# Performance work log

Measured on AMD Instinct MI355X. Metric: run time of the kernel, lower is better.

## Reference

```python
import jax, jax.numpy as jnp
import numpy as np

B, S, N, D, H = 128, 512, 32, 512, 2  # batch, seq_len, num_size, node_dim, hop_size
NPAD = 4  # padded number slots per row


def _lin(key, fi, fo):
    return 0.02 * jax.random.normal(key, (H, fi, fo), jnp.float32), jnp.zeros((H, fo), jnp.float32)


def setup_inputs() -> dict:
    key = jax.random.key(0)
    ks = jax.random.split(key, 12)
    encoder_outputs = jax.random.normal(ks[0], (S, B, D), jnp.float32)
    num_encoder_outputs = jax.random.normal(ks[1], (B, N, D), jnp.float32)
    # distinct positions per row in [0, S), last NPAD slots padded with -1
    num_pos_pad = jnp.argsort(jax.random.uniform(ks[2], (B, S)), axis=-1)[:, :N].astype(jnp.int32)
    num_pos_pad = num_pos_pad.at[:, -NPAD:].set(-1)
    # order ranks 1..N (random permutation per row), 0 on padded slots
    num_order_pad = (jnp.argsort(jax.random.uniform(ks[3], (B, N)), axis=-1) + 1).astype(jnp.int32)
    num_order_pad = num_order_pad.at[:, -NPAD:].set(0)
    w_n1a, b_n1a = _lin(ks[4], D, D)
    w_n1b, b_n1b = _lin(ks[5], D, D)
    w_n2a, b_n2a = _lin(ks[6], D, D)
    w_n2b, b_n2b = _lin(ks[7], D, D)
    w_g, b_g = _lin(ks[8], 4 * D, D)
    w_o, b_o = _lin(ks[9], 2 * D, D)
    return dict(encoder_outputs=encoder_outputs, num_encoder_outputs=num_encoder_outputs,
                num_pos_pad=num_pos_pad, num_order_pad=num_order_pad,
                w_n1a=w_n1a, b_n1a=b_n1a, w_n1b=w_n1b, b_n1b=b_n1b,
                w_n2a=w_n2a, b_n2a=b_n2a, w_n2b=w_n2b, b_n2b=b_n2b,
                w_g=w_g, b_g=b_g, w_o=w_o, b_o=b_o)


def reference(encoder_outputs, num_encoder_outputs, num_pos_pad, num_order_pad,
              w_n1a, b_n1a, w_n1b, b_n1b, w_n2a, b_n2a, w_n2b, b_n2b,
              w_g, b_g, w_o, b_o):
    node_mask = (num_order_pad > 0)                              # [B,N]
    greater = num_order_pad[:, :, None] > num_order_pad[:, None, :]
    lower = ~greater                                             # <=
    eye = jnp.eye(N, dtype=jnp.float32)
    pair = (node_mask[:, None, :] & node_mask[:, :, None]).astype(jnp.float32) * (1.0 - eye)
    g_gt = pair * greater.astype(jnp.float32) + eye              # [B,N,N]
    g_lt = pair * lower.astype(jnp.float32) + eye
    # row-normalize (D^{-1} A); diagonal guarantees row sums >= 1
    g_gt = g_gt / g_gt.sum(-1, keepdims=True)
    g_lt = g_lt / g_lt.sum(-1, keepdims=True)

    node = num_encoder_outputs                                   # [B,N,D]
    for h in range(H):
        ni1 = jax.nn.relu(jnp.einsum('bnm,bmd,de->bne', g_gt, node, w_n1a[h]) + b_n1a[h])
        ni1 = jax.nn.relu(jnp.einsum('bnm,bmd,de->bne', g_gt, ni1, w_n1b[h]) + b_n1b[h])
        ni2 = jax.nn.relu(jnp.einsum('bnm,bmd,de->bne', g_lt, node, w_n2a[h]) + b_n2a[h])
        ni2 = jax.nn.relu(jnp.einsum('bnm,bmd,de->bne', g_lt, ni2, w_n2b[h]) + b_n2b[h])
        gate_in = jnp.concatenate([ni1, ni2, ni1 + ni2, ni1 - ni2], axis=-1)
        gate = jax.nn.sigmoid(gate_in @ w_g[h] + b_g[h])
        node_info = gate * ni1 + (1.0 - gate) * ni2
        node = jax.nn.relu(jnp.concatenate([node, node_info], axis=-1) @ w_o[h] + b_o[h])

    # scatter node embeddings into padded [B, S+1, D]; pads -> slot S (dropped)
    num_mask = num_pos_pad > -1
    clamped = jnp.where(num_mask, num_pos_pad, S)                # [B,N]
    gnn_info = jnp.zeros((B, S + 1, D), jnp.float32)
    gnn_info = gnn_info.at[jnp.arange(B)[:, None], clamped].set(node)
    gnn_info = gnn_info[:, :S, :].transpose(1, 0, 2)             # [S,B,D]
    gnn_info = encoder_outputs + gnn_info
    num_embedding = num_encoder_outputs + node
    problem_output = jnp.max(gnn_info, axis=0)                   # [B,D]
    return gnn_info, num_embedding, problem_output
```

## Files before the change

### kernel.cpp

```cpp
#include <hip/hip_runtime.h>
#include <math.h>

#define BB 128
#define SS 512
#define NN 32
#define DD 512
#define HH 2
#define MM (BB * NN)
#define DSQ (DD * DD)

typedef short bf16x8 __attribute__((ext_vector_type(8)));
typedef float f32x4 __attribute__((ext_vector_type(4)));

__device__ __forceinline__ unsigned short f2bf(float f) {
    unsigned int u = __float_as_uint(f);
    u += 0x7fffu + ((u >> 16) & 1u);
    return (unsigned short)(u >> 16);
}
__device__ __forceinline__ float bf2f(unsigned short h) {
    return __uint_as_float(((unsigned int)h) << 16);
}
__device__ __forceinline__ void g2l16(const void* gp, void* lp) {
    __builtin_amdgcn_global_load_lds(
        (const __attribute__((address_space(1))) void*)gp,
        (__attribute__((address_space(3))) void*)lp, 16, 0, 0);
}

__global__ __launch_bounds__(256) void adj_k(const int* __restrict__ order,
                                             const int* __restrict__ pos,
                                             float* __restrict__ g_gt,
                                             float* __restrict__ g_lt,
                                             int* __restrict__ slot) {
    int b = blockIdx.x;
    __shared__ int ord[NN];
    __shared__ float sgt[NN][NN + 1];
    __shared__ float slt[NN][NN + 1];
    __shared__ float rs_gt[NN], rs_lt[NN];
    int tid = threadIdx.x;
    slot[b * SS + tid] = -1;
    slot[b * SS + 256 + tid] = -1;
    if (tid < NN) ord[tid] = order[b * NN + tid];
    __syncthreads();
    for (int q = 0; q < 4; ++q) {
        int idx = tid + 256 * q;
        int n = idx >> 5, m = idx & 31;
        bool valid = (ord[n] > 0) && (ord[m] > 0) && (n != m);
        float eye = (n == m) ? 1.f : 0.f;
        bool gt = ord[n] > ord[m];
        sgt[n][m] = ((valid && gt) ? 1.f : 0.f) + eye;
        slt[n][m] = ((valid && !gt) ? 1.f : 0.f) + eye;
    }
    __syncthreads();
    if (tid < NN) {
        float s1 = 0.f, s2 = 0.f;
        for (int m = 0; m < NN; ++m) { s1 += sgt[tid][m]; s2 += slt[tid][m]; }
        rs_gt[tid] = s1; rs_lt[tid] = s2;
    }
    __syncthreads();
    for (int q = 0; q < 4; ++q) {
        int idx = tid + 256 * q;
        int n = idx >> 5, m = idx & 31;
        g_gt[b * 1024 + idx] = sgt[n][m] / rs_gt[n];
        g_lt[b * 1024 + idx] = slt[n][m] / rs_lt[n];
    }
    if (tid < NN) {
        int p = pos[b * NN + tid];
        if (p >= 0) slot[b * SS + p] = tid;
    }
}

struct WSfull { const float* s[12]; int slot[12]; const float* w_g; };

__global__ __launch_bounds__(256) void wprep_k(WSfull w, unsigned short* __restrict__ Wt) {
    int which = blockIdx.x;
    int tile = blockIdx.y;
    int tr = (tile >> 3) * 64, tc = (tile & 7) * 64;
    __shared__ float c1[64][65];
    __shared__ float c2[64][65];
    int lc = threadIdx.x & 63, g4 = threadIdx.x >> 6;
    if (which < 12) {
        const float* src = w.s[which];
        unsigned short* dst = Wt + (size_t)w.slot[which] * DSQ;
        for (int i = 0; i < 16; ++i) {
            int lr = g4 * 16 + i;
            c1[lr][lc] = src[(size_t)(tr + lr) * DD + tc + lc];
        }
        __syncthreads();
        for (int i = 0; i < 16; ++i) {
            int lr = g4 * 16 + i;
            dst[(size_t)(tc + lr) * DD + tr + lc] = f2bf(c1[lc][lr]);
        }
    } else {
        int h = which - 12;
        const float* base = w.w_g + (size_t)h * 4 * DSQ;
        for (int i = 0; i < 16; ++i) {
            int lr = g4 * 16 + i;
            int k = tr + lr, n = tc + lc;
            float a  = base[(size_t)k * DD + n];
            float b2 = base[(size_t)(DD + k) * DD + n];
            float c  = base[(size_t)(2 * DD + k) * DD + n];
            float d4 = base[(size_t)(3 * DD + k) * DD + n];
            c1[lr][lc] = a + c + d4;
            c2[lr][lc] = b2 + c - d4;
        }
        __syncthreads();
        unsigned short* d1 = Wt + (size_t)(h * 8 + 4) * DSQ;
        unsigned short* d2 = Wt + (size_t)(h * 8 + 5) * DSQ;
        for (int i = 0; i < 16; ++i) {
            int lr = g4 * 16 + i;
            d1[(size_t)(tc + lr) * DD + tr + lc] = f2bf(c1[lc][lr]);
            d2[(size_t)(tc + lr) * DD + tr + lc] = f2bf(c2[lc][lr]);
        }
    }
}

__global__ __launch_bounds__(256) void convmix_k(const float* __restrict__ x,
                                                 const float* __restrict__ g_gt,
                                                 const float* __restrict__ g_lt,
                                                 unsigned short* __restrict__ node0,
                                                 unsigned short* __restrict__ t1,
                                                 unsigned short* __restrict__ t2) {
    const int b = blockIdx.x;
    const int dc = blockIdx.y * 128;
    __shared__ float xs[NN][128];
    __shared__ float gg[2][NN][NN];
    const int t = threadIdx.x;
    ((float4*)gg)[t]       = ((const float4*)(g_gt + (size_t)b * 1024))[t];
    ((float4*)gg)[t + 256] = ((const float4*)(g_lt + (size_t)b * 1024))[t];
#pragma unroll
    for (int q = 0; q < 4; ++q) {
        int e = t + 256 * q;
        int row = e >> 5, c4 = (e & 31) * 4;
        float4 v = *(const float4*)(x + (size_t)(b * NN + row) * DD + dc + c4);
        *(float4*)&xs[row][c4] = v;
        ushort4 o;
        o.x = f2bf(v.x); o.y = f2bf(v.y); o.z = f2bf(v.z); o.w = f2bf(v.w);
        *(ushort4*)(node0 + (size_t)(b * NN + row) * DD + dc + c4) = o;
    }
    __syncthreads();
#pragma unroll
    for (int gi = 0; gi < 2; ++gi) {
        unsigned short* O = gi ? t2 : t1;
#pragma unroll
        for (int it = 0; it < 4; ++it) {
            int task = it * 256 + t;
            int n = task >> 5, dq = task & 31;
            f32x4 r = {0.f, 0.f, 0.f, 0.f};
#pragma unroll
            for (int m = 0; m < NN; ++m)
                r += gg[gi][n][m] * *(const f32x4*)(&xs[m][dq * 4]);
            ushort4 ov;
            ov.x = f2bf(r.x); ov.y = f2bf(r.y); ov.z = f2bf(r.z); ov.w = f2bf(r.w);
            *(ushort4*)(O + (size_t)(b * NN + n) * DD + dc + dq * 4) = ov;
        }
    }
}

struct GA {
    const unsigned short* A1; const unsigned short* W1;
    const unsigned short* A2; const unsigned short* W2;
    const float* bias;
    const unsigned short* gin1; const unsigned short* gin2;
    const float* G1; const float* G2;
    unsigned short* out; unsigned short* out2; unsigned short* out3;
};

template <bool DUAL, bool GATE, int EMIX>
__global__ __launch_bounds__(256) void mgemm_k(GA a0, GA a1) {
    GA g = (blockIdx.z == 0) ? a0 : a1;
    constexpr int LDSB = 49152 + (EMIX == 1 ? 8192 : EMIX == 2 ? 16384 : 0);
    __shared__ __align__(16) char lds[LDSB];
    unsigned short* Ab = (unsigned short*)lds;
    unsigned short* Bb = (unsigned short*)(lds + 16384);
    float* gsh = (float*)(lds + 49152);
    const int tid = threadIdx.x;
    const int lane = tid & 63;
    const int wave = tid >> 6;
    const int wr = wave & 1, wc = wave >> 1;
    const int bm = blockIdx.x * 64, bn = blockIdx.y * 128;

    if (EMIX >= 1) {
        const float4* g1 = (const float4*)(g.G1 + (size_t)(bm >> 5) * 1024);
        ((float4*)gsh)[tid] = g1[tid];
        ((float4*)gsh)[tid + 256] = g1[tid + 256];
        if (EMIX == 2) {
            const float4* g2v = (const float4*)(g.G2 + (size_t)(bm >> 5) * 1024);
            ((float4*)(gsh + 2048))[tid] = g2v[tid];
            ((float4*)(gsh + 2048))[tid + 256] = g2v[tid + 256];
        }
    }

    f32x4 acc[2][4];
#pragma unroll
    for (int i = 0; i < 2; ++i)
#pragma unroll
        for (int j = 0; j < 4; ++j) {
            acc[i][j].x = 0.f; acc[i][j].y = 0.f; acc[i][j].z = 0.f; acc[i][j].w = 0.f;
        }

    const int rA0 = tid >> 3,          sA0 = (tid & 7) ^ (rA0 & 7);
    const int rA1 = (tid + 256) >> 3,  sA1 = (tid & 7) ^ (rA1 & 7);
    int rB[4], sB[4];
#pragma unroll
    for (int q = 0; q < 4; ++q) {
        int e = tid + 256 * q;
        rB[q] = e >> 3;
        sB[q] = (tid & 7) ^ (rB[q] & 7);
    }

    int aoff[2][2], boff[2][4];
#pragma unroll
    for (int t = 0; t < 2; ++t) {
        int sl = t * 4 + (lane >> 4);
        int p = sl ^ (lane & 7);
#pragma unroll
        for (int i = 0; i < 2; ++i) {
            int m = wr * 32 + i * 16 + (lane & 15);
            aoff[t][i] = m * 64 + p * 8;
        }
#pragma unroll
        for (int j = 0; j < 4; ++j) {
            int n = wc * 64 + j * 16 + (lane & 15);
            boff[t][j] = n * 64 + p * 8;
        }
    }

    auto STAGE = [&](int ks, int c) {
        const unsigned short* A = (DUAL && ks >= 8) ? g.A2 : g.A1;
        const unsigned short* W = (DUAL && ks >= 8) ? g.W2 : g.W1;
        const int k0 = (ks & 7) * 64;
        g2l16(A + (size_t)(bm + rA0) * DD + k0 + sA0 * 8, Ab + c * 4096 + tid * 8);
        g2l16(A + (size_t)(bm + rA1) * DD + k0 + sA1 * 8,
              Ab + c * 4096 + (tid + 256) * 8);
#pragma unroll
        for (int q = 0; q < 4; ++q)
            g2l16(W + (size_t)(bn + rB[q]) * DD + k0 + sB[q] * 8,
                  Bb + c * 8192 + (tid + 256 * q) * 8);
    };

    const int NK = DUAL ? 16 : 8;
    STAGE(0, 0);
    __syncthreads();
    int cur = 0;
    for (int ks = 0; ks < NK; ++ks) {
        if (ks + 1 < NK) STAGE(ks + 1, cur ^ 1);
        const unsigned short* Ac = Ab + cur * 4096;
        const unsigned short* Bc = Bb + cur * 8192;
        bf16x8 af[2][2], bf_[2][4];
#pragma unroll
        for (int t = 0; t < 2; ++t) {
#pragma unroll
            for (int i = 0; i < 2; ++i) af[t][i] = *(const bf16x8*)(Ac + aoff[t][i]);
#pragma unroll
            for (int j = 0; j < 4; ++j) bf_[t][j] = *(const bf16x8*)(Bc + boff[t][j]);
        }
#pragma unroll
        for (int t = 0; t < 2; ++t)
#pragma unroll
            for (int i = 0; i < 2; ++i)
#pragma unroll
                for (int j = 0; j < 4; ++j)
                    acc[i][j] = __builtin_amdgcn_mfma_f32_16x16x32_bf16(
                        af[t][i], bf_[t][j], acc[i][j], 0, 0, 0);
        __syncthreads();
        cur ^= 1;
    }

    if (EMIX == 0) {
#pragma unroll
        for (int i = 0; i < 2; ++i) {
            int row = bm + wr * 32 + i * 16 + (lane >> 4) * 4;
#pragma unroll
            for (int j = 0; j < 4; ++j) {
                int col = bn + wc * 64 + j * 16 + (lane & 15);
                float bv = g.bias[col];
#pragma unroll
                for (int rg = 0; rg < 4; ++rg) {
                    float v = acc[i][j][rg] + bv;
                    size_t idx = (size_t)(row + rg) * DD + col;
                    if (GATE) {
                        float gg = 1.f / (1.f + __expf(-v));
                        float x1 = bf2f(g.gin1[idx]);
                        float x2 = bf2f(g.gin2[idx]);
                        g.out[idx] = f2bf(gg * x1 + (1.f - gg) * x2);
                    } else {
                        g.out[idx] = f2bf(fmaxf(v, 0.f));
                    }
                }
            }
        }
    } else {
        float* S = (float*)lds;
#pragma unroll
        for (int i = 0; i < 2; ++i) {
            int lrow = wr * 32 + i * 16 + (lane >> 4) * 4;
#pragma unroll
            for (int j = 0; j < 4; ++j) {
                int lcol = wc * 64 + j * 16 + (lane & 15);
                float bv = g.bias[bn + lcol];
#pragma unroll
                for (int rg = 0; rg < 4; ++rg) {
                    float v = fmaxf(acc[i][j][rg] + bv, 0.f);
                    S[(lrow + rg) * 128 + lcol] = v;
                    if (EMIX == 2)
                        g.out[(size_t)(bm + lrow + rg) * DD + bn + lcol] = f2bf(v);
                }
            }
        }
        __syncthreads();
        const int ngi = (EMIX == 2) ? 2 : 1;
#pragma unroll
        for (int gi = 0; gi < ngi; ++gi) {
            unsigned short* O = (EMIX == 2) ? (gi ? g.out3 : g.out2) : g.out;
            const float* gb = gsh + gi * 2048;
#pragma unroll
            for (int it = 0; it < 8; ++it) {
                int task = it * 256 + tid;
                int n = task >> 5, dq = task & 31;
                int bt = n >> 5, nl = n & 31;
                const float* gr = gb + bt * 1024 + nl * 32;
                const float* Sb = S + bt * 32 * 128 + dq * 4;
                f32x4 r = {0.f, 0.f, 0.f, 0.f};
#pragma unroll
                for (int m = 0; m < NN; ++m)
                    r += gr[m] * *(const f32x4*)(Sb + m * 128);
                ushort4 ov;
                ov.x = f2bf(r.x); ov.y = f2bf(r.y); ov.z = f2bf(r.z); ov.w = f2bf(r.w);
                *(ushort4*)(O + (size_t)(bm + n) * DD + bn + dq * 4) = ov;
            }
        }
    }
}

__global__ __launch_bounds__(256) void gnn_k(const float* __restrict__ enc,
                                             const unsigned short* __restrict__ node,
                                             const int* __restrict__ slot,
                                             const float* __restrict__ num_enc,
                                             float* __restrict__ out_gnn,
                                             float* __restrict__ out_nemb,
                                             float* __restrict__ partial) {
    int b = blockIdx.x;
    int t = threadIdx.x;
    if (blockIdx.y >= 16) {
        int q = blockIdx.y - 16;
        size_t base = (size_t)b * NN * DD + (size_t)q * (NN * DD / 4);
        for (int it = 0; it < 4; ++it) {
            size_t i = base + (size_t)(it * 256 + t) * 4;
            float4 a = *(const float4*)(num_enc + i);
            ushort4 nb = *(const ushort4*)(node + i);
            float4 r;
            r.x = a.x + bf2f(nb.x);
            r.y = a.y + bf2f(nb.y);
            r.z = a.z + bf2f(nb.z);
            r.w = a.w + bf2f(nb.w);
            *(float4*)(out_nemb + i) = r;
        }
        return;
    }
    __shared__ int sl[32];
    __shared__ float4 red[128];
    int s0 = blockIdx.y * 32;
    if (t < 32) sl[t] = slot[b * SS + s0 + t];
    __syncthreads();
    const int dv = (t & 127) * 4;
    const int sh = t >> 7;
    float4 mx = {-INFINITY, -INFINITY, -INFINITY, -INFINITY};
#pragma unroll 4
    for (int i = 0; i < 16; ++i) {
        int sloc = sh * 16 + i;
        int s = s0 + sloc;
        int n = sl[sloc];
        size_t ebase = ((size_t)s * BB + b) * DD + dv;
        float4 v = *(const float4*)(enc + ebase);
        if (n >= 0) {
            ushort4 nb = *(const ushort4*)(node + ((size_t)b * NN + n) * DD + dv);
            v.x += bf2f(nb.x);
            v.y += bf2f(nb.y);
            v.z += bf2f(nb.z);
            v.w += bf2f(nb.w);
        }
        *(float4*)(out_gnn + ebase) = v;
        mx.x = fmaxf(mx.x, v.x);
        mx.y = fmaxf(mx.y, v.y);
        mx.z = fmaxf(mx.z, v.z);
        mx.w = fmaxf(mx.w, v.w);
    }
    if (sh == 1) red[t & 127] = mx;
    __syncthreads();
    if (sh == 0) {
        float4 o = red[t];
        mx.x = fmaxf(mx.x, o.x);
        mx.y = fmaxf(mx.y, o.y);
        mx.z = fmaxf(mx.z, o.z);
        mx.w = fmaxf(mx.w, o.w);
        *(float4*)(partial + ((size_t)b * 16 + blockIdx.y) * DD + dv) = mx;
    }
}

__global__ void pmax_k(const float* __restrict__ partial, float* __restrict__ out_prob) {
    int i = blockIdx.x * 256 + threadIdx.x;
    if (i >= BB * DD) return;
    int b = i >> 9, d = i & 511;
    float m = -INFINITY;
    for (int c = 0; c < 16; ++c) m = fmaxf(m, partial[((size_t)b * 16 + c) * DD + d]);
    out_prob[i] = m;
}

extern "C" void kernel_launch(void* const* d_in, const int* in_sizes, int n_in,
                              void* d_out, int out_size, void* d_ws, size_t ws_size,
                              hipStream_t stream) {
    const float* enc     = (const float*)d_in[0];
    const float* num_enc = (const float*)d_in[1];
    const int*   pos     = (const int*)d_in[2];
    const int*   order   = (const int*)d_in[3];
    const float* w_n1a = (const float*)d_in[4];  const float* b_n1a = (const float*)d_in[5];
    const float* w_n1b = (const float*)d_in[6];  const float* b_n1b = (const float*)d_in[7];
    const float* w_n2a = (const float*)d_in[8];  const float* b_n2a = (const float*)d_in[9];
    const float* w_n2b = (const float*)d_in[10]; const float* b_n2b = (const float*)d_in[11];
    const float* w_g   = (const float*)d_in[12]; const float* b_g   = (const float*)d_in[13];
    const float* w_o   = (const float*)d_in[14]; const float* b_o   = (const float*)d_in[15];

    char* wp = (char*)d_ws;
    float* g_gt = (float*)wp;        wp += (size_t)BB * NN * NN * 4;
    float* g_lt = (float*)wp;        wp += (size_t)BB * NN * NN * 4;
    float* partial = (float*)wp;     wp += (size_t)BB * 16 * DD * 4;
    int* slot = (int*)wp;            wp += (size_t)BB * SS * 4;
    unsigned short* Wt = (unsigned short*)wp;    wp += (size_t)16 * DSQ * 2;
    unsigned short* node0 = (unsigned short*)wp; wp += (size_t)MM * DD * 2;
    unsigned short* nodeA = (unsigned short*)wp; wp += (size_t)MM * DD * 2;
    unsigned short* nodeB = (unsigned short*)wp; wp += (size_t)MM * DD * 2;
    unsigned short* ni1 = (unsigned short*)wp;   wp += (size_t)MM * DD * 2;
    unsigned short* ni2 = (unsigned short*)wp;   wp += (size_t)MM * DD * 2;
    unsigned short* t1 = (unsigned short*)wp;    wp += (size_t)MM * DD * 2;
    unsigned short* t2 = (unsigned short*)wp;    wp += (size_t)MM * DD * 2;

    float* out_gnn  = (float*)d_out;
    float* out_nemb = out_gnn + (size_t)SS * BB * DD;
    float* out_prob = out_nemb + (size_t)BB * NN * DD;

    adj_k<<<BB, 256, 0, stream>>>(order, pos, g_gt, g_lt, slot);

    WSfull wsrc;
    const float* srcs[12] = {w_n1a, w_n1b, w_n2a, w_n2b, w_o, w_o + DSQ,
                             w_n1a + DSQ, w_n1b + DSQ, w_n2a + DSQ, w_n2b + DSQ,
                             w_o + 2 * DSQ, w_o + 3 * DSQ};
    int slots[12] = {0, 1, 2, 3, 6, 7, 8, 9, 10, 11, 14, 15};
    for (int i = 0; i < 12; ++i) { wsrc.s[i] = srcs[i]; wsrc.slot[i] = slots[i]; }
    wsrc.w_g = w_g;
    wprep_k<<<dim3(14, 64), 256, 0, stream>>>(wsrc, Wt);
    convmix_k<<<dim3(BB, 4), 256, 0, stream>>>(num_enc, g_gt, g_lt, node0, t1, t2);

    dim3 ggrid(MM / 64, DD / 128, 2);
    dim3 sgrid(MM / 64, DD / 128, 1);

    for (int h = 0; h < HH; ++h) {
        const unsigned short* Wh = Wt + (size_t)h * 8 * DSQ;
        const unsigned short* nodeIn = (h == 0) ? node0 : nodeA;

        GA sa0 = {t1, Wh + 0 * DSQ, nullptr, nullptr, b_n1a + h * DD,
                  nullptr, nullptr, g_gt, nullptr, ni1, nullptr, nullptr};
        GA sa1 = {t2, Wh + 2 * DSQ, nullptr, nullptr, b_n2a + h * DD,
                  nullptr, nullptr, g_lt, nullptr, ni2, nullptr, nullptr};
        mgemm_k<false, false, 1><<<ggrid, 256, 0, stream>>>(sa0, sa1);

        GA sb0 = {ni1, Wh + 1 * DSQ, nullptr, nullptr, b_n1b + h * DD,
                  nullptr, nullptr, nullptr, nullptr, t1, nullptr, nullptr};
        GA sb1 = {ni2, Wh + 3 * DSQ, nullptr, nullptr, b_n2b + h * DD,
                  nullptr, nullptr, nullptr, nullptr, t2, nullptr, nullptr};
        mgemm_k<false, false, 0><<<ggrid, 256, 0, stream>>>(sb0, sb1);

        GA gg2 = {t1, Wh + 4 * DSQ, t2, Wh + 5 * DSQ, b_g + h * DD,
                  t1, t2, nullptr, nullptr, ni1, nullptr, nullptr};
        mgemm_k<true, true, 0><<<sgrid, 256, 0, stream>>>(gg2, gg2);

        if (h == 0) {
            GA go = {nodeIn, Wh + 6 * DSQ, ni1, Wh + 7 * DSQ, b_o + h * DD,
                     nullptr, nullptr, g_gt, g_lt, nodeA, t1, t2};
            mgemm_k<true, false, 2><<<sgrid, 256, 0, stream>>>(go, go);
        } else {
            GA go = {nodeIn, Wh + 6 * DSQ, ni1, Wh + 7 * DSQ, b_o + h * DD,
                     nullptr, nullptr, nullptr, nullptr, nodeB, nullptr, nullptr};
            mgemm_k<true, false, 0><<<sgrid, 256, 0, stream>>>(go, go);
        }
    }
    const unsigned short* nodeF = nodeB;

    gnn_k<<<dim3(BB, 20), 256, 0, stream>>>(enc, nodeF, slot, num_enc,
                                            out_gnn, out_nemb, partial);
    pmax_k<<<(BB * DD) / 256, 256, 0, stream>>>(partial, out_prob);
}
```

Baseline: 423.8 us.

## Fuse all post-prep stages into a persistent kernel with software grid barriers

Replaces the convmix, eight GEMM launches, gnn and pmax kernels with one persistent 512-block kernel. The stages are separated by an atomic-counter grid barrier, and the barrier counter is reset inside adj_k. The goal is to remove per-launch overhead and tail gaps between the many small dependent kernels. In exchange, half of the blocks sit idle during the dual-GEMM stages, and the kernel relies on all 512 blocks being co-resident, or it will deadlock. Occupancy is also limited by the 64KB of LDS per block.

```diff
diff --git a/kernel.cpp b/kernel.cpp
--- a/kernel.cpp
+++ b/kernel.cpp
@@ -8,6 +8,7 @@
 #define HH 2
 #define MM (BB * NN)
 #define DSQ (DD * DD)
+#define NBLK 512u
 
 typedef short bf16x8 __attribute__((ext_vector_type(8)));
 typedef float f32x4 __attribute__((ext_vector_type(4)));
@@ -26,17 +27,31 @@
         (__attribute__((address_space(3))) void*)lp, 16, 0, 0);
 }
 
+__device__ __forceinline__ void gridbar(unsigned int* bar) {
+    __syncthreads();
+    if (threadIdx.x == 0) {
+        __threadfence();
+        unsigned int old = atomicAdd(bar, 1u);
+        unsigned int target = (old / NBLK + 1u) * NBLK;
+        while (atomicAdd(bar, 0u) < target) __builtin_amdgcn_s_sleep(1);
+        __threadfence();
+    }
+    __syncthreads();
+}
+
 __global__ __launch_bounds__(256) void adj_k(const int* __restrict__ order,
                                              const int* __restrict__ pos,
                                              float* __restrict__ g_gt,
                                              float* __restrict__ g_lt,
-                                             int* __restrict__ slot) {
+                                             int* __restrict__ slot,
+                                             unsigned int* __restrict__ bar) {
     int b = blockIdx.x;
     __shared__ int ord[NN];
     __shared__ float sgt[NN][NN + 1];
     __shared__ float slt[NN][NN + 1];
     __shared__ float rs_gt[NN], rs_lt[NN];
     int tid = threadIdx.x;
+    if (b == 0 && tid == 0) *bar = 0u;
     slot[b * SS + tid] = -1;
     slot[b * SS + 256 + tid] = -1;
     if (tid < NN) ord[tid] = order[b * NN + tid];
@@ -114,48 +129,6 @@
     }
 }
 
-__global__ __launch_bounds__(256) void convmix_k(const float* __restrict__ x,
-                                                 const float* __restrict__ g_gt,
-                                                 const float* __restrict__ g_lt,
-                                                 unsigned short* __restrict__ node0,
-                                                 unsigned short* __restrict__ t1,
-                                                 unsigned short* __restrict__ t2) {
-    const int b = blockIdx.x;
-    const int dc = blockIdx.y * 128;
-    __shared__ float xs[NN][128];
-    __shared__ float gg[2][NN][NN];
-    const int t = threadIdx.x;
-    ((float4*)gg)[t]       = ((const float4*)(g_gt + (size_t)b * 1024))[t];
-    ((float4*)gg)[t + 256] = ((const float4*)(g_lt + (size_t)b * 1024))[t];
-#pragma unroll
-    for (int q = 0; q < 4; ++q) {
-        int e = t + 256 * q;
-        int row = e >> 5, c4 = (e & 31) * 4;
-        float4 v = *(const float4*)(x + (size_t)(b * NN + row) * DD + dc + c4);
-        *(float4*)&xs[row][c4] = v;
-        ushort4 o;
-        o.x = f2bf(v.x); o.y = f2bf(v.y); o.z = f2bf(v.z); o.w = f2bf(v.w);
-        *(ushort4*)(node0 + (size_t)(b * NN + row) * DD + dc + c4) = o;
-    }
-    __syncthreads();
-#pragma unroll
-    for (int gi = 0; gi < 2; ++gi) {
-        unsigned short* O = gi ? t2 : t1;
-#pragma unroll
-        for (int it = 0; it < 4; ++it) {
-            int task = it * 256 + t;
-            int n = task >> 5, dq = task & 31;
-            f32x4 r = {0.f, 0.f, 0.f, 0.f};
-#pragma unroll
-            for (int m = 0; m < NN; ++m)
-                r += gg[gi][n][m] * *(const f32x4*)(&xs[m][dq * 4]);
-            ushort4 ov;
-            ov.x = f2bf(r.x); ov.y = f2bf(r.y); ov.z = f2bf(r.z); ov.w = f2bf(r.w);
-            *(ushort4*)(O + (size_t)(b * NN + n) * DD + dc + dq * 4) = ov;
-        }
-    }
-}
-
 struct GA {
     const unsigned short* A1; const unsigned short* W1;
     const unsigned short* A2; const unsigned short* W2;
@@ -166,10 +139,8 @@
 };
 
 template <bool DUAL, bool GATE, int EMIX>
-__global__ __launch_bounds__(256) void mgemm_k(GA a0, GA a1) {
-    GA g = (blockIdx.z == 0) ? a0 : a1;
-    constexpr int LDSB = 49152 + (EMIX == 1 ? 8192 : EMIX == 2 ? 16384 : 0);
-    __shared__ __align__(16) char lds[LDSB];
+__device__ __forceinline__ void gemm_tile(const GA& g, const int bm, const int bn,
+                                          char* lds) {
     unsigned short* Ab = (unsigned short*)lds;
     unsigned short* Bb = (unsigned short*)(lds + 16384);
     float* gsh = (float*)(lds + 49152);
@@ -177,7 +148,8 @@
     const int lane = tid & 63;
     const int wave = tid >> 6;
     const int wr = wave & 1, wc = wave >> 1;
-    const int bm = blockIdx.x * 64, bn = blockIdx.y * 128;
+
+    __syncthreads();
 
     if (EMIX >= 1) {
         const float4* g1 = (const float4*)(g.G1 + (size_t)(bm >> 5) * 1024);
@@ -332,78 +304,191 @@
     }
 }
 
-__global__ __launch_bounds__(256) void gnn_k(const float* __restrict__ enc,
-                                             const unsigned short* __restrict__ node,
-                                             const int* __restrict__ slot,
-                                             const float* __restrict__ num_enc,
-                                             float* __restrict__ out_gnn,
-                                             float* __restrict__ out_nemb,
-                                             float* __restrict__ partial) {
-    int b = blockIdx.x;
-    int t = threadIdx.x;
-    if (blockIdx.y >= 16) {
-        int q = blockIdx.y - 16;
-        size_t base = (size_t)b * NN * DD + (size_t)q * (NN * DD / 4);
-        for (int it = 0; it < 4; ++it) {
-            size_t i = base + (size_t)(it * 256 + t) * 4;
-            float4 a = *(const float4*)(num_enc + i);
-            ushort4 nb = *(const ushort4*)(node + i);
-            float4 r;
-            r.x = a.x + bf2f(nb.x);
-            r.y = a.y + bf2f(nb.y);
-            r.z = a.z + bf2f(nb.z);
-            r.w = a.w + bf2f(nb.w);
-            *(float4*)(out_nemb + i) = r;
-        }
-        return;
-    }
-    __shared__ int sl[32];
-    __shared__ float4 red[128];
-    int s0 = blockIdx.y * 32;
-    if (t < 32) sl[t] = slot[b * SS + s0 + t];
-    __syncthreads();
-    const int dv = (t & 127) * 4;
-    const int sh = t >> 7;
-    float4 mx = {-INFINITY, -INFINITY, -INFINITY, -INFINITY};
+struct MegaA {
+    const float* num_enc;
+    const float *g_gt, *g_lt;
+    unsigned short *node0, *nodeA, *nodeB, *t1, *t2, *ni1, *ni2;
+    const unsigned short* Wt;
+    const float *b_n1a, *b_n1b, *b_n2a, *b_n2b, *b_g, *b_o;
+    const float* enc;
+    const int* slot;
+    float *out_gnn, *out_nemb, *partial, *out_prob;
+    unsigned int* bar;
+};
+
+__global__ __launch_bounds__(256, 2) void mega_k(MegaA a) {
+    __shared__ __align__(16) char lds[65536];
+    const int bid = blockIdx.x;
+    const int tid = threadIdx.x;
+    const int tile = bid & 255;
+    const int bm = (tile >> 2) * 64, bn = (tile & 3) * 128;
+
+    {
+        float* xs = (float*)lds;
+        float* gg = (float*)(lds + 16384);
+        const int b = bid >> 2;
+        const int dc = (bid & 3) * 128;
+        ((float4*)gg)[tid]       = ((const float4*)(a.g_gt + (size_t)b * 1024))[tid];
+        ((float4*)gg)[tid + 256] = ((const float4*)(a.g_lt + (size_t)b * 1024))[tid];
+#pragma unroll
+        for (int q = 0; q < 4; ++q) {
+            int e = tid + 256 * q;
+            int row = e >> 5, c4 = (e & 31) * 4;
+            float4 v = *(const float4*)(a.num_enc + (size_t)(b * NN + row) * DD + dc + c4);
+            *(float4*)&xs[row * 128 + c4] = v;
+            ushort4 o;
+            o.x = f2bf(v.x); o.y = f2bf(v.y); o.z = f2bf(v.z); o.w = f2bf(v.w);
+            *(ushort4*)(a.node0 + (size_t)(b * NN + row) * DD + dc + c4) = o;
+        }
+        __syncthreads();
+#pragma unroll
+        for (int gi = 0; gi < 2; ++gi) {
+            unsigned short* O = gi ? a.t2 : a.t1;
+#pragma unroll
+            for (int it = 0; it < 4; ++it) {
+                int task = it * 256 + tid;
+                int n = task >> 5, dq = task & 31;
+                f32x4 r = {0.f, 0.f, 0.f, 0.f};
+#pragma unroll
+                for (int m = 0; m < NN; ++m)
+                    r += gg[gi * 1024 + n * 32 + m] * *(const f32x4*)(&xs[m * 128 + dq * 4]);
+                ushort4 ov;
+                ov.x = f2bf(r.x); ov.y = f2bf(r.y); ov.z = f2bf(r.z); ov.w = f2bf(r.w);
+                *(ushort4*)(O + (size_t)(b * NN + n) * DD + dc + dq * 4) = ov;
+            }
+        }
+    }
+    gridbar(a.bar);
+
+    for (int h = 0; h < HH; ++h) {
+        const unsigned short* Wh = a.Wt + (size_t)h * 8 * DSQ;
+        const unsigned short* nodeIn = (h == 0) ? a.node0 : a.nodeA;
+        unsigned short* nodeOut = (h == 0) ? a.nodeA : a.nodeB;
+
+        {
+            GA g = {};
+            if (bid < 256) {
+                g.A1 = a.t1; g.W1 = Wh + 0 * DSQ; g.bias = a.b_n1a + h * DD;
+                g.G1 = a.g_gt; g.out = a.ni1;
+            } else {
+                g.A1 = a.t2; g.W1 = Wh + 2 * DSQ; g.bias = a.b_n2a + h * DD;
+                g.G1 = a.g_lt; g.out = a.ni2;
+            }
+            gemm_tile<false, false, 1>(g, bm, bn, lds);
+        }
+        gridbar(a.bar);
+
+        {
+            GA g = {};
+            if (bid < 256) {
+                g.A1 = a.ni1; g.W1 = Wh + 1 * DSQ; g.bias = a.b_n1b + h * DD;
+                g.out = a.t1;
+            } else {
+                g.A1 = a.ni2; g.W1 = Wh + 3 * DSQ; g.bias = a.b_n2b + h * DD;
+                g.out = a.t2;
+            }
+            gemm_tile<false, false, 0>(g, bm, bn, lds);
+        }
+        gridbar(a.bar);
+
+        if (bid < 256) {
+            GA g = {};
+            g.A1 = a.t1; g.W1 = Wh + 4 * DSQ; g.A2 = a.t2; g.W2 = Wh + 5 * DSQ;
+            g.bias = a.b_g + h * DD; g.gin1 = a.t1; g.gin2 = a.t2; g.out = a.ni1;
+            gemm_tile<true, true, 0>(g, bm, bn, lds);
+        }
+        gridbar(a.bar);
+
+        if (bid < 256) {
+            if (h == 0) {
+                GA g = {};
+                g.A1 = nodeIn; g.W1 = Wh + 6 * DSQ; g.A2 = a.ni1; g.W2 = Wh + 7 * DSQ;
+                g.bias = a.b_o + h * DD;
+                g.G1 = a.g_gt; g.G2 = a.g_lt;
+                g.out = nodeOut; g.out2 = a.t1; g.out3 = a.t2;
+                gemm_tile<true, false, 2>(g, bm, bn, lds);
+            } else {
+                GA g = {};
+                g.A1 = nodeIn; g.W1 = Wh + 6 * DSQ; g.A2 = a.ni1; g.W2 = Wh + 7 * DSQ;
+                g.bias = a.b_o + h * DD; g.out = nodeOut;
+                gemm_tile<true, false, 0>(g, bm, bn, lds);
+            }
+        }
+        gridbar(a.bar);
+    }
+
+    {
+        int* sl = (int*)lds;
+        float4* red = (float4*)(lds + 256);
+        const unsigned short* node = a.nodeB;
+        for (int u = 0; u < 5; ++u) {
+            __syncthreads();
+            int unit = bid * 5 + u;
+            int b = unit / 20, y = unit % 20;
+            if (y >= 16) {
+                int q = y - 16;
+                size_t base = (size_t)b * NN * DD + (size_t)q * (NN * DD / 4);
+                for (int it = 0; it < 4; ++it) {
+                    size_t i = base + (size_t)(it * 256 + tid) * 4;
+                    float4 av = *(const float4*)(a.num_enc + i);
+                    ushort4 nb = *(const ushort4*)(node + i);
+                    float4 r;
+                    r.x = av.x + bf2f(nb.x);
+                    r.y = av.y + bf2f(nb.y);
+                    r.z = av.z + bf2f(nb.z);
+                    r.w = av.w + bf2f(nb.w);
+                    *(float4*)(a.out_nemb + i) = r;
+                }
+                continue;
+            }
+            int s0 = y * 32;
+            if (tid < 32) sl[tid] = a.slot[b * SS + s0 + tid];
+            __syncthreads();
+            const int dv = (tid & 127) * 4;
+            const int sh = tid >> 7;
+            float4 mx = {-INFINITY, -INFINITY, -INFINITY, -INFINITY};
 #pragma unroll 4
-    for (int i = 0; i < 16; ++i) {
-        int sloc = sh * 16 + i;
-        int s = s0 + sloc;
-        int n = sl[sloc];
-        size_t ebase = ((size_t)s * BB + b) * DD + dv;
-        float4 v = *(const float4*)(enc + ebase);
-        if (n >= 0) {
-            ushort4 nb = *(const ushort4*)(node + ((size_t)b * NN + n) * DD + dv);
-            v.x += bf2f(nb.x);
-            v.y += bf2f(nb.y);
-            v.z += bf2f(nb.z);
-            v.w += bf2f(nb.w);
-        }
-        *(float4*)(out_gnn + ebase) = v;
-        mx.x = fmaxf(mx.x, v.x);
-        mx.y = fmaxf(mx.y, v.y);
-        mx.z = fmaxf(mx.z, v.z);
-        mx.w = fmaxf(mx.w, v.w);
-    }
-    if (sh == 1) red[t & 127] = mx;
-    __syncthreads();
-    if (sh == 0) {
-        float4 o = red[t];
-        mx.x = fmaxf(mx.x, o.x);
-        mx.y = fmaxf(mx.y, o.y);
-        mx.z = fmaxf(mx.z, o.z);
-        mx.w = fmaxf(mx.w, o.w);
-        *(float4*)(partial + ((size_t)b * 16 + blockIdx.y) * DD + dv) = mx;
-    }
-}
-
-__global__ void pmax_k(const float* __restrict__ partial, float* __restrict__ out_prob) {
-    int i = blockIdx.x * 256 + threadIdx.x;
-    if (i >= BB * DD) return;
-    int b = i >> 9, d = i & 511;
-    float m = -INFINITY;
-    for (int c = 0; c < 16; ++c) m = fmaxf(m, partial[((size_t)b * 16 + c) * DD + d]);
-    out_prob[i] = m;
+            for (int i = 0; i < 16; ++i) {
+                int sloc = sh * 16 + i;
+                int s = s0 + sloc;
+                int n = sl[sloc];
+                size_t ebase = ((size_t)s * BB + b) * DD + dv;
+                float4 v = *(const float4*)(a.enc + ebase);
+                if (n >= 0) {
+                    ushort4 nb = *(const ushort4*)(node + ((size_t)b * NN + n) * DD + dv);
+                    v.x += bf2f(nb.x);
+                    v.y += bf2f(nb.y);
+                    v.z += bf2f(nb.z);
+                    v.w += bf2f(nb.w);
+                }
+                *(float4*)(a.out_gnn + ebase) = v;
+                mx.x = fmaxf(mx.x, v.x);
+                mx.y = fmaxf(mx.y, v.y);
+                mx.z = fmaxf(mx.z, v.z);
+                mx.w = fmaxf(mx.w, v.w);
+            }
+            if (sh == 1) red[tid & 127] = mx;
+            __syncthreads();
+            if (sh == 0) {
+                float4 o = red[tid];
+                mx.x = fmaxf(mx.x, o.x);
+                mx.y = fmaxf(mx.y, o.y);
+                mx.z = fmaxf(mx.z, o.z);
+                mx.w = fmaxf(mx.w, o.w);
+                *(float4*)(a.partial + ((size_t)b * 16 + y) * DD + dv) = mx;
+            }
+        }
+    }
+    gridbar(a.bar);
+
+    if (tid < 128) {
+        int i = bid * 128 + tid;
+        int b = i >> 9, d = i & 511;
+        float m = -INFINITY;
+        for (int c = 0; c < 16; ++c)
+            m = fmaxf(m, a.partial[((size_t)b * 16 + c) * DD + d]);
+        a.out_prob[i] = m;
+    }
 }
 
 extern "C" void kernel_launch(void* const* d_in, const int* in_sizes, int n_in,
@@ -425,6 +510,7 @@
     float* g_lt = (float*)wp;        wp += (size_t)BB * NN * NN * 4;
     float* partial = (float*)wp;     wp += (size_t)BB * 16 * DD * 4;
     int* slot = (int*)wp;            wp += (size_t)BB * SS * 4;
+    unsigned int* bar = (unsigned int*)wp;       wp += 256;
     unsigned short* Wt = (unsigned short*)wp;    wp += (size_t)16 * DSQ * 2;
     unsigned short* node0 = (unsigned short*)wp; wp += (size_t)MM * DD * 2;
     unsigned short* nodeA = (unsigned short*)wp; wp += (size_t)MM * DD * 2;
@@ -438,7 +524,7 @@
     float* out_nemb = out_gnn + (size_t)SS * BB * DD;
     float* out_prob = out_nemb + (size_t)BB * NN * DD;
 
-    adj_k<<<BB, 256, 0, stream>>>(order, pos, g_gt, g_lt, slot);
+    adj_k<<<BB, 256, 0, stream>>>(order, pos, g_gt, g_lt, slot, bar);
 
     WSfull wsrc;
     const float* srcs[12] = {w_n1a, w_n1b, w_n2a, w_n2b, w_o, w_o + DSQ,
@@ -448,44 +534,17 @@
     for (int i = 0; i < 12; ++i) { wsrc.s[i] = srcs[i]; wsrc.slot[i] = slots[i]; }
     wsrc.w_g = w_g;
     wprep_k<<<dim3(14, 64), 256, 0, stream>>>(wsrc, Wt);
-    convmix_k<<<dim3(BB, 4), 256, 0, stream>>>(num_enc, g_gt, g_lt, node0, t1, t2);
-
-    dim3 ggrid(MM / 64, DD / 128, 2);
-    dim3 sgrid(MM / 64, DD / 128, 1);
-
-    for (int h = 0; h < HH; ++h) {
-        const unsigned short* Wh = Wt + (size_t)h * 8 * DSQ;
-        const unsigned short* nodeIn = (h == 0) ? node0 : nodeA;
-
-        GA sa0 = {t1, Wh + 0 * DSQ, nullptr, nullptr, b_n1a + h * DD,
-                  nullptr, nullptr, g_gt, nullptr, ni1, nullptr, nullptr};
-        GA sa1 = {t2, Wh + 2 * DSQ, nullptr, nullptr, b_n2a + h * DD,
-                  nullptr, nullptr, g_lt, nullptr, ni2, nullptr, nullptr};
-        mgemm_k<false, false, 1><<<ggrid, 256, 0, stream>>>(sa0, sa1);
-
-        GA sb0 = {ni1, Wh + 1 * DSQ, nullptr, nullptr, b_n1b + h * DD,
-                  nullptr, nullptr, nullptr, nullptr, t1, nullptr, nullptr};
-        GA sb1 = {ni2, Wh + 3 * DSQ, nullptr, nullptr, b_n2b + h * DD,
-                  nullptr, nullptr, nullptr, nullptr, t2, nullptr, nullptr};
-        mgemm_k<false, false, 0><<<ggrid, 256, 0, stream>>>(sb0, sb1);
-
-        GA gg2 = {t1, Wh + 4 * DSQ, t2, Wh + 5 * DSQ, b_g + h * DD,
-                  t1, t2, nullptr, nullptr, ni1, nullptr, nullptr};
-        mgemm_k<true, true, 0><<<sgrid, 256, 0, stream>>>(gg2, gg2);
-
-        if (h == 0) {
-            GA go = {nodeIn, Wh + 6 * DSQ, ni1, Wh + 7 * DSQ, b_o + h * DD,
-                     nullptr, nullptr, g_gt, g_lt, nodeA, t1, t2};
-            mgemm_k<true, false, 2><<<sgrid, 256, 0, stream>>>(go, go);
-        } else {
-            GA go = {nodeIn, Wh + 6 * DSQ, ni1, Wh + 7 * DSQ, b_o + h * DD,
-                     nullptr, nullptr, nullptr, nullptr, nodeB, nullptr, nullptr};
-            mgemm_k<true, false, 0><<<sgrid, 256, 0, stream>>>(go, go);
-        }
-    }
-    const unsigned short* nodeF = nodeB;
-
-    gnn_k<<<dim3(BB, 20), 256, 0, stream>>>(enc, nodeF, slot, num_enc,
-                                            out_gnn, out_nemb, partial);
-    pmax_k<<<(BB * DD) / 256, 256, 0, stream>>>(partial, out_prob);
-}
+
+    MegaA ma;
+    ma.num_enc = num_enc; ma.g_gt = g_gt; ma.g_lt = g_lt;
+    ma.node0 = node0; ma.nodeA = nodeA; ma.nodeB = nodeB;
+    ma.t1 = t1; ma.t2 = t2; ma.ni1 = ni1; ma.ni2 = ni2;
+    ma.Wt = Wt;
+    ma.b_n1a = b_n1a; ma.b_n1b = b_n1b; ma.b_n2a = b_n2a; ma.b_n2b = b_n2b;
+    ma.b_g = b_g; ma.b_o = b_o;
+    ma.enc = enc; ma.slot = slot;
+    ma.out_gnn = out_gnn; ma.out_nemb = out_nemb;
+    ma.partial = partial; ma.out_prob = out_prob;
+    ma.bar = bar;
+    mega_k<<<NBLK, 256, 0, stream>>>(ma);
+}
```

New measurement: 971.1 us. 2.29x slower.
